# Kernel optimization log

Measured on AMD Instinct MI355X. Metric: run time of the kernel, lower is better.

Reference implementation:

```python
import jax, jax.numpy as jnp
import numpy as np

NEG = jnp.float32(-1e9)  # -inf surrogate, safe for logsumexp
EPS = 1e-7               # keras.backend.epsilon()


def _ctc_loss(y_true, y_pred):
    """Faithful K.ctc_batch_cost with full input/label lengths.

    y_true: [B, L] int labels in [0, C-2] (blank = C-1, TF convention)
    y_pred: [B, T, C] softmax probabilities
    returns: [B, 1] negative log-likelihood per sample
    """
    B, T, C = y_pred.shape
    L = y_true.shape[1]
    blank = C - 1
    S = 2 * L + 1  # extended label: blank-interleaved

    logp = jnp.log(y_pred + EPS)  # [B, T, C]

    # Extended label sequence [blank, l1, blank, l2, ..., lL, blank]
    ext = jnp.full((B, S), blank, dtype=jnp.int32).at[:, 1::2].set(
        y_true.astype(jnp.int32))  # [B, S]

    # Skip transition (s-2 -> s) allowed iff ext[s] != blank and ext[s] != ext[s-2]
    skip = jnp.concatenate(
        [jnp.zeros((B, 2), dtype=bool),
         (ext[:, 2:] != blank) & (ext[:, 2:] != ext[:, :-2])],
        axis=1)  # [B, S]

    # Gather lattice log-probs once: [B, T, S]
    lp = jnp.take_along_axis(logp, ext[:, None, :], axis=2)

    # alpha at t=0: only states 0 (blank) and 1 (first label) reachable
    alpha0 = jnp.full((B, S), NEG).at[:, 0].set(lp[:, 0, 0]).at[:, 1].set(lp[:, 0, 1])

    def step(alpha, lp_t):
        a1 = alpha                                                     # stay
        a2 = jnp.pad(alpha[:, :-1], ((0, 0), (1, 0)), constant_values=NEG)  # advance 1
        a3 = jnp.pad(alpha[:, :-2], ((0, 0), (2, 0)), constant_values=NEG)  # advance 2
        a3 = jnp.where(skip, a3, NEG)
        new = lp_t + jax.nn.logsumexp(jnp.stack([a1, a2, a3]), axis=0)
        return new, None

    lp_rest = jnp.transpose(lp[:, 1:, :], (1, 0, 2))  # [T-1, B, S]
    alphaT, _ = jax.lax.scan(step, alpha0, lp_rest)

    # Total log-prob ends in last blank or last label
    ll = jax.nn.logsumexp(alphaT[:, S - 2:S], axis=1)  # [B]
    return -ll[:, None]  # [B, 1], matches ctc_batch_cost's expand_dims


def setup_inputs() -> dict:
    key = jax.random.key(0)
    k1, k2 = jax.random.split(key)
    B, T, C, L = 512, 512, 128, 64
    logits = jax.random.normal(k1, (B, T, C), dtype=jnp.float32)
    y_pred = jax.nn.softmax(logits, axis=-1)  # ctc_batch_cost expects probs
    y_true = jax.random.randint(k2, (B, L), 0, C - 1)  # labels exclude blank C-1
    return {"y_true": y_true, "y_pred": y_pred}


def reference(y_true, y_pred):
    return _ctc_loss(y_true, y_pred)
```

## Files before the change

### kernel.cpp

```cpp
#include <hip/hip_runtime.h>


constexpr int Tn = 512;
constexpr int Cn = 128;
constexpr int Ln = 64;
constexpr float NEGF = -1e9f;
constexpr float EPSF = 1e-7f;
constexpr float LN2F = 0.6931471805599453f;

#if __has_builtin(__builtin_amdgcn_exp2f)
#define EXP2F(x) __builtin_amdgcn_exp2f(x)
#else
#define EXP2F(x) __expf((x) * 0.6931471805599453f)
#endif
#if __has_builtin(__builtin_amdgcn_logf)
#define LOG2F(x) __builtin_amdgcn_logf(x)
#else
#define LOG2F(x) (__logf(x) * 1.4426950408889634f)
#endif

__global__ __launch_bounds__(64)
void ctc_fwd(const int* __restrict__ y_true,
             const float* __restrict__ y_pred,
             float* __restrict__ out)
{
    const int b    = blockIdx.x;
    const int lane = threadIdx.x;

    const float2* row = (const float2*)(y_pred + (size_t)b * Tn * Cn);

    const int  lab   = y_true[b * Ln + lane];
    const int  labp  = __shfl_up(lab, 1, 64);
    const bool skip  = (lane > 0) && (lab != labp);
    const int  baddr = (lab >> 1) << 2;
    const bool bhi   = (lab & 1) != 0;

    auto lp_pair = [&](float2 p, float& lpb, float& lpl) {
        float pb = __shfl(p.y, 63, 64);
        lpb = LOG2F(pb + EPSF);
        int lo = __builtin_amdgcn_ds_bpermute(baddr, __float_as_int(p.x));
        int hi = __builtin_amdgcn_ds_bpermute(baddr, __float_as_int(p.y));
        float pl = bhi ? __int_as_float(hi) : __int_as_float(lo);
        lpl = LOG2F(pl + EPSF);
    };

    float2 p0 = row[lane];
    float2 pv[8];
    #pragma unroll
    for (int k = 0; k < 8; ++k) pv[k] = row[(k + 1) * 64 + lane];

    float a0, a1, aX;
    {
        float lpb, lpl;
        lp_pair(p0, lpb, lpl);
        a0 = (lane == 0) ? lpb : NEGF;
        a1 = (lane == 0) ? lpl : NEGF;
        aX = NEGF;
    }

    auto step = [&](float2 p) {
        float lpb, lpl;
        lp_pair(p, lpb, lpl);
        float up1 = __shfl_up(a1, 1, 64);
        if (lane == 0) up1 = NEGF;
        float m0 = fmaxf(a0, up1);
        float n0 = lpb + m0 + LOG2F(EXP2F(a0 - m0) + EXP2F(up1 - m0));
        float a3 = skip ? up1 : NEGF;
        float m1 = fmaxf(fmaxf(a1, a0), a3);
        float n1 = lpl + m1 +
                   LOG2F(EXP2F(a1 - m1) + EXP2F(a0 - m1) + EXP2F(a3 - m1));
        float mX = fmaxf(aX, a1);
        float nX = lpb + mX + LOG2F(EXP2F(aX - mX) + EXP2F(a1 - mX));
        a0 = n0; a1 = n1; aX = nX;
    };

    for (int tb = 1; tb <= 497; tb += 8) {
        #pragma unroll
        for (int u = 0; u < 8; ++u) {
            step(pv[u]);
            int tn = tb + u + 8;
            tn = tn > 511 ? 511 : tn;
            pv[u] = row[tn * 64 + lane];
        }
    }
    #pragma unroll
    for (int u = 0; u < 7; ++u) step(pv[u]);

    if (lane == 63) {
        float m  = fmaxf(a1, aX);
        float ll = m + LOG2F(EXP2F(a1 - m) + EXP2F(aX - m));
        out[b] = -ll * LN2F;
    }
}

extern "C" void kernel_launch(void* const* d_in, const int* in_sizes, int n_in,
                              void* d_out, int out_size, void* d_ws, size_t ws_size,
                              hipStream_t stream)
{
    const int*   y_true = (const int*)d_in[0];
    const float* y_pred = (const float*)d_in[1];
    float*       out    = (float*)d_out;

    const int B = out_size;
    ctc_fwd<<<dim3(B), dim3(64), 0, stream>>>(y_true, y_pred, out);
}
```

Measured before the change: 235.0 us.

## Software-pipeline CTC lattice log-prob prep and use DPP shifts for alpha recurrence

Splits each time step into stages: logs and bpermute gathers for future steps are computed several iterations ahead, so the serial alpha recurrence no longer waits on LDS permute latency. The per-lane state is re-mapped so that lane 0's leading blank chain is tracked as a scalar-like running sum (aZ), and the blank-state logsumexp is simplified to a two-term max/min form. Cross-lane shifts use a DPP row shift instead of a shfl_up, and the prefetch depth grows to 16 rows. The cost is more registers and more complex indexing. The DPP row shift 0x138 may not cross 16-lane row boundaries, which is a correctness risk.

```diff
diff --git a/kernel.cpp b/kernel.cpp
--- a/kernel.cpp
+++ b/kernel.cpp
@@ -8,16 +8,13 @@
 constexpr float EPSF = 1e-7f;
 constexpr float LN2F = 0.6931471805599453f;
 
-#if __has_builtin(__builtin_amdgcn_exp2f)
 #define EXP2F(x) __builtin_amdgcn_exp2f(x)
-#else
-#define EXP2F(x) __expf((x) * 0.6931471805599453f)
-#endif
-#if __has_builtin(__builtin_amdgcn_logf)
 #define LOG2F(x) __builtin_amdgcn_logf(x)
-#else
-#define LOG2F(x) (__logf(x) * 1.4426950408889634f)
-#endif
+
+__device__ __forceinline__ float dpp_shr1(float x) {
+    return __int_as_float(__builtin_amdgcn_update_dpp(
+        0, __float_as_int(x), 0x138 , 0xF, 0xF, true));
+}
 
 __global__ __launch_bounds__(64)
 void ctc_fwd(const int* __restrict__ y_true,
@@ -27,70 +24,99 @@
     const int b    = blockIdx.x;
     const int lane = threadIdx.x;
 
-    const float2* row = (const float2*)(y_pred + (size_t)b * Tn * Cn);
+    const float2* __restrict__ row = (const float2*)(y_pred + (size_t)b * Tn * Cn);
 
     const int  lab   = y_true[b * Ln + lane];
     const int  labp  = __shfl_up(lab, 1, 64);
     const bool skip  = (lane > 0) && (lab != labp);
     const int  baddr = (lab >> 1) << 2;
     const bool bhi   = (lab & 1) != 0;
+    const bool l0    = (lane == 0);
 
-    auto lp_pair = [&](float2 p, float& lpb, float& lpl) {
-        float pb = __shfl(p.y, 63, 64);
-        lpb = LOG2F(pb + EPSF);
-        int lo = __builtin_amdgcn_ds_bpermute(baddr, __float_as_int(p.x));
-        int hi = __builtin_amdgcn_ds_bpermute(baddr, __float_as_int(p.y));
-        float pl = bhi ? __int_as_float(hi) : __int_as_float(lo);
-        lpl = LOG2F(pl + EPSF);
+    float2 pv[16];
+    float  bpLo[4], bpHi[4];
+    float  lpLv[4];
+    float  lpbv[8];
+
+    float aA, aB, aZ;
+
+    float2 p0 = row[lane];
+    #pragma unroll
+    for (int k = 0; k < 16; ++k) pv[k] = row[(1 + k) * 64 + lane];
+
+    {
+        float g0 = LOG2F(p0.x + EPSF);
+        float g1 = LOG2F(p0.y + EPSF);
+        aZ = __int_as_float(__builtin_amdgcn_readlane(__float_as_int(g1), 63));
+        float bl = __int_as_float(__builtin_amdgcn_ds_bpermute(baddr, __float_as_int(g0)));
+        float bh = __int_as_float(__builtin_amdgcn_ds_bpermute(baddr, __float_as_int(g1)));
+        float lpl0 = bhi ? bh : bl;
+        aA = l0 ? lpl0 : NEGF;
+        aB = NEGF;
+    }
+
+    #pragma unroll
+    for (int j = 0; j < 8; ++j) {
+        float g0 = LOG2F(pv[j].x + EPSF);
+        float g1 = LOG2F(pv[j].y + EPSF);
+        lpbv[j] = __int_as_float(__builtin_amdgcn_readlane(__float_as_int(g1), 63));
+        float bl = __int_as_float(__builtin_amdgcn_ds_bpermute(baddr, __float_as_int(g0)));
+        float bh = __int_as_float(__builtin_amdgcn_ds_bpermute(baddr, __float_as_int(g1)));
+        if (j < 4) lpLv[j] = bhi ? bh : bl;
+        else { bpLo[j - 4] = bl; bpHi[j - 4] = bh; }
+    }
+
+    auto consume = [&](int u) {
+        float lpb = lpbv[u & 7];
+        float lpl = lpLv[u & 3];
+        float upA = dpp_shr1(aA);
+        float upB = dpp_shr1(aB);
+        upA = l0 ? NEGF : upA;
+        upB = l0 ? aZ   : upB;
+        float a3 = skip ? upA : NEGF;
+        float m1 = fmaxf(fmaxf(aA, upB), a3);
+        float s1 = EXP2F(aA - m1) + EXP2F(upB - m1) + EXP2F(a3 - m1);
+        float nA = lpl + m1 + LOG2F(s1);
+        float m2 = fmaxf(aB, aA);
+        float n2 = fminf(aB, aA);
+        float nB = lpb + m2 + LOG2F(1.0f + EXP2F(n2 - m2));
+        aZ += lpb;
+        aA = nA; aB = nB;
+    };
+    auto stageB = [&](int u) {
+        lpLv[u & 3] = bhi ? bpHi[u & 3] : bpLo[u & 3];
+    };
+    auto stageA = [&](int u) {
+        float2 p = pv[(u + 8) & 15];
+        float g0 = LOG2F(p.x + EPSF);
+        float g1 = LOG2F(p.y + EPSF);
+        lpbv[u & 7] = __int_as_float(__builtin_amdgcn_readlane(__float_as_int(g1), 63));
+        bpLo[u & 3] = __int_as_float(__builtin_amdgcn_ds_bpermute(baddr, __float_as_int(g0)));
+        bpHi[u & 3] = __int_as_float(__builtin_amdgcn_ds_bpermute(baddr, __float_as_int(g1)));
     };
 
-    float2 p0 = row[lane];
-    float2 pv[8];
-    #pragma unroll
-    for (int k = 0; k < 8; ++k) pv[k] = row[(k + 1) * 64 + lane];
-
-    float a0, a1, aX;
-    {
-        float lpb, lpl;
-        lp_pair(p0, lpb, lpl);
-        a0 = (lane == 0) ? lpb : NEGF;
-        a1 = (lane == 0) ? lpl : NEGF;
-        aX = NEGF;
-    }
-
-    auto step = [&](float2 p) {
-        float lpb, lpl;
-        lp_pair(p, lpb, lpl);
-        float up1 = __shfl_up(a1, 1, 64);
-        if (lane == 0) up1 = NEGF;
-        float m0 = fmaxf(a0, up1);
-        float n0 = lpb + m0 + LOG2F(EXP2F(a0 - m0) + EXP2F(up1 - m0));
-        float a3 = skip ? up1 : NEGF;
-        float m1 = fmaxf(fmaxf(a1, a0), a3);
-        float n1 = lpl + m1 +
-                   LOG2F(EXP2F(a1 - m1) + EXP2F(a0 - m1) + EXP2F(a3 - m1));
-        float mX = fmaxf(aX, a1);
-        float nX = lpb + mX + LOG2F(EXP2F(aX - mX) + EXP2F(a1 - mX));
-        a0 = n0; a1 = n1; aX = nX;
-    };
-
-    for (int tb = 1; tb <= 497; tb += 8) {
+    int t = 1;
+    for (int blk = 0; blk < 31; ++blk) {
         #pragma unroll
-        for (int u = 0; u < 8; ++u) {
-            step(pv[u]);
-            int tn = tb + u + 8;
-            tn = tn > 511 ? 511 : tn;
-            pv[u] = row[tn * 64 + lane];
+        for (int u = 0; u < 16; ++u, ++t) {
+            consume(u);
+            stageB(u);
+            stageA(u);
+            int rn = t + 16; rn = rn > 511 ? 511 : rn;
+            pv[u] = row[rn * 64 + lane];
         }
     }
     #pragma unroll
-    for (int u = 0; u < 7; ++u) step(pv[u]);
+    for (int u = 0; u < 15; ++u, ++t) {
+        consume(u);
+        stageB(u);
+        stageA(u);
+    }
 
-    if (lane == 63) {
-        float m  = fmaxf(a1, aX);
-        float ll = m + LOG2F(EXP2F(a1 - m) + EXP2F(aX - m));
-        out[b] = -ll * LN2F;
-    }
+    float m  = fmaxf(aA, aB);
+    float n  = fminf(aA, aB);
+    float ll = m + LOG2F(1.0f + EXP2F(n - m));
+    if (lane == 63) out[b] = -ll * LN2F;
 }
 
 extern "C" void kernel_launch(void* const* d_in, const int* in_sizes, int n_in,
```

Result: faster. 210.9 us (-10.3%).

## Run CTC recursion in linear probability space with periodic power-of-two rescaling

Applied to the files above, without the earlier changes.

Replaces the log-space logsumexp recursion with a linear-space forward pass: multiply-add on probabilities plus a wave-wide max reduction every 8 steps that rescales by a power of two and tracks the exponent shift. Label and blank probabilities are loaded per lane by direct scalar gathers into a 32-deep register prefetch ring, instead of float2 rows with bpermute/shfl. Lane shifts use DPP moves instead of ds_bpermute-based shuffles. This removes most exp/log transcendentals and LDS-permute traffic from the serial time loop, at the cost of possible underflow between rescales and more register pressure.

```diff
diff --git a/kernel.cpp b/kernel.cpp
--- a/kernel.cpp
+++ b/kernel.cpp
@@ -1,23 +1,14 @@
 #include <hip/hip_runtime.h>
 
 
-constexpr int Tn = 512;
-constexpr int Cn = 128;
-constexpr int Ln = 64;
-constexpr float NEGF = -1e9f;
 constexpr float EPSF = 1e-7f;
 constexpr float LN2F = 0.6931471805599453f;
 
-#if __has_builtin(__builtin_amdgcn_exp2f)
-#define EXP2F(x) __builtin_amdgcn_exp2f(x)
-#else
-#define EXP2F(x) __expf((x) * 0.6931471805599453f)
-#endif
-#if __has_builtin(__builtin_amdgcn_logf)
-#define LOG2F(x) __builtin_amdgcn_logf(x)
-#else
-#define LOG2F(x) (__logf(x) * 1.4426950408889634f)
-#endif
+template<int CTRL>
+__device__ __forceinline__ float dpp_mov(float x) {
+    return __int_as_float(__builtin_amdgcn_update_dpp(
+        0, __float_as_int(x), CTRL, 0xF, 0xF, true));
+}
 
 __global__ __launch_bounds__(64)
 void ctc_fwd(const int* __restrict__ y_true,
@@ -27,70 +18,89 @@
     const int b    = blockIdx.x;
     const int lane = threadIdx.x;
 
-    const float2* row = (const float2*)(y_pred + (size_t)b * Tn * Cn);
+    const char* __restrict__ base =
+        (const char*)(y_pred + (size_t)b * 512 * 128);
 
-    const int  lab   = y_true[b * Ln + lane];
-    const int  labp  = __shfl_up(lab, 1, 64);
-    const bool skip  = (lane > 0) && (lab != labp);
-    const int  baddr = (lab >> 1) << 2;
-    const bool bhi   = (lab & 1) != 0;
+    const int   lab   = y_true[b * 64 + lane];
+    const int   labp  = __shfl_up(lab, 1, 64);
+    const float skipf = (lane > 0 && lab != labp) ? 1.0f : 0.0f;
+    const bool  l0    = (lane == 0);
 
-    auto lp_pair = [&](float2 p, float& lpb, float& lpl) {
-        float pb = __shfl(p.y, 63, 64);
-        lpb = LOG2F(pb + EPSF);
-        int lo = __builtin_amdgcn_ds_bpermute(baddr, __float_as_int(p.x));
-        int hi = __builtin_amdgcn_ds_bpermute(baddr, __float_as_int(p.y));
-        float pl = bhi ? __int_as_float(hi) : __int_as_float(lo);
-        lpl = LOG2F(pl + EPSF);
+    const int offL = lab * 4;
+    const int offB = 127 * 4;
+
+    float pLab[32], pBlank[32];
+
+    #pragma unroll
+    for (int r = 0; r < 32; ++r) {
+        pLab[r]   = *(const float*)(base + r * 512 + offL);
+        pBlank[r] = *(const float*)(base + r * 512 + offB);
+    }
+
+    float aZ, aA, aB;
+    {
+        float pb0 = pBlank[0] + EPSF;
+        float pl0 = pLab[0]   + EPSF;
+        aZ = pb0;
+        aA = l0 ? pl0 : 0.0f;
+        aB = 0.0f;
+    }
+
+    int   shift = 0;
+    float red   = 0.0f;
+
+    auto slot = [&](int t, int u, bool doLoad) {
+        float pl = pLab[u]   + EPSF;
+        float pb = pBlank[u] + EPSF;
+        float upA = dpp_mov<0x138>(aA);
+        float upB = dpp_mov<0x138>(aB);
+        upB = l0 ? aZ : upB;
+        float ts = aA + upB;
+        ts = fmaf(skipf, upA, ts);
+        float nA = pl * ts;
+        float nB = pb * (aB + aA);
+        aZ *= pb;
+        aA = nA; aB = nB;
+
+        if ((u & 7) == 3) {
+            float r = fmaxf(fmaxf(aA, aB), aZ);
+            r = fmaxf(r, dpp_mov<0x111>(r));
+            r = fmaxf(r, dpp_mov<0x112>(r));
+            r = fmaxf(r, dpp_mov<0x114>(r));
+            r = fmaxf(r, dpp_mov<0x118>(r));
+            r = fmaxf(r, dpp_mov<0x142>(r));
+            r = fmaxf(r, dpp_mov<0x143>(r));
+            red = r;
+        }
+        if ((u & 7) == 7) {
+            int mb = __builtin_amdgcn_readlane(__float_as_int(red), 63);
+            int e  = (mb >> 23) & 0xff;
+            int f  = 314 - e;
+            f = f < 1 ? 1 : (f > 254 ? 254 : f);
+            float scale = __int_as_float(f << 23);
+            shift += f - 127;
+            aA *= scale; aB *= scale; aZ *= scale;
+        }
+        if (doLoad) {
+            int rn = t + 32; rn = rn > 511 ? 511 : rn;
+            pLab[u]   = *(const float*)(base + rn * 512 + offL);
+            pBlank[u] = *(const float*)(base + rn * 512 + offB);
+        }
     };
 
-    float2 p0 = row[lane];
-    float2 pv[8];
-    #pragma unroll
-    for (int k = 0; k < 8; ++k) pv[k] = row[(k + 1) * 64 + lane];
-
-    float a0, a1, aX;
-    {
-        float lpb, lpl;
-        lp_pair(p0, lpb, lpl);
-        a0 = (lane == 0) ? lpb : NEGF;
-        a1 = (lane == 0) ? lpl : NEGF;
-        aX = NEGF;
-    }
-
-    auto step = [&](float2 p) {
-        float lpb, lpl;
-        lp_pair(p, lpb, lpl);
-        float up1 = __shfl_up(a1, 1, 64);
-        if (lane == 0) up1 = NEGF;
-        float m0 = fmaxf(a0, up1);
-        float n0 = lpb + m0 + LOG2F(EXP2F(a0 - m0) + EXP2F(up1 - m0));
-        float a3 = skip ? up1 : NEGF;
-        float m1 = fmaxf(fmaxf(a1, a0), a3);
-        float n1 = lpl + m1 +
-                   LOG2F(EXP2F(a1 - m1) + EXP2F(a0 - m1) + EXP2F(a3 - m1));
-        float mX = fmaxf(aX, a1);
-        float nX = lpb + mX + LOG2F(EXP2F(aX - mX) + EXP2F(a1 - mX));
-        a0 = n0; a1 = n1; aX = nX;
-    };
-
-    for (int tb = 1; tb <= 497; tb += 8) {
+    for (int blk = 0; blk < 15; ++blk) {
+        int t0 = 1 + blk * 32;
         #pragma unroll
-        for (int u = 0; u < 8; ++u) {
-            step(pv[u]);
-            int tn = tb + u + 8;
-            tn = tn > 511 ? 511 : tn;
-            pv[u] = row[tn * 64 + lane];
-        }
+        for (int i = 0; i < 32; ++i)
+            slot(t0 + i, (1 + i) & 31, true);
     }
     #pragma unroll
-    for (int u = 0; u < 7; ++u) step(pv[u]);
+    for (int i = 0; i < 31; ++i)
+        slot(481 + i, (482 + i - 1) & 31, false);
 
-    if (lane == 63) {
-        float m  = fmaxf(a1, aX);
-        float ll = m + LOG2F(EXP2F(a1 - m) + EXP2F(aX - m));
-        out[b] = -ll * LN2F;
-    }
+    float s   = aA + aB;
+    float ll2 = __builtin_amdgcn_logf(s);
+    if (lane == 63) out[b] = ((float)shift - ll2) * LN2F;
 }
 
 extern "C" void kernel_launch(void* const* d_in, const int* in_sizes, int n_in,
```

Result: faster. 191.7 us (-18.4%).
